# Performance work log

Measured on AMD Instinct MI355X. Metric: run time of the kernel, lower is better.

Reference implementation:

```python
import jax, jax.numpy as jnp
import numpy as np


def setup_inputs() -> dict:
    key = jax.random.key(0)
    ks = jax.random.split(key, 4)
    B, S, H = 1, 2048, 2048
    E, I = 32, 768
    scale_h = 1.0 / np.sqrt(H)
    scale_i = 1.0 / np.sqrt(I)
    return {
        "hidden_states": jax.random.normal(ks[0], (B, S, H), dtype=jnp.float32),
        "gate_w": jax.random.normal(ks[1], (E, H), dtype=jnp.float32) * scale_h,
        "gate_up_proj": jax.random.normal(ks[2], (E, H, 2 * I), dtype=jnp.float32) * scale_h,
        "down_proj": jax.random.normal(ks[3], (E, I, H), dtype=jnp.float32) * scale_i,
    }


TOP_K = 4


def reference(hidden_states, gate_w, gate_up_proj, down_proj):
    B, S, H = hidden_states.shape
    x = hidden_states.reshape(-1, H)                      # [T, H]
    T = x.shape[0]

    # Router: softmax -> top-k -> renormalize -> scatter back to dense [T, E]
    router_logits = x @ gate_w.T                          # [T, E]
    probs = jax.nn.softmax(router_logits.astype(jnp.float32), axis=-1)
    top_w, top_idx = jax.lax.top_k(probs, TOP_K)          # [T, K]
    top_w = top_w / jnp.sum(top_w, axis=-1, keepdims=True)
    top_w = top_w.astype(x.dtype)
    router_weights = jnp.zeros_like(router_logits).at[
        jnp.arange(T)[:, None], top_idx
    ].set(top_w)                                          # [T, E]

    # Experts (eval path): every expert processes every token, then weight & sum.
    gate_up = jnp.einsum("th,ehi->eti", x, gate_up_proj)  # [E, T, 2I]
    gate, up = jnp.split(gate_up, 2, axis=-1)
    h = up * jax.nn.silu(gate)                            # [E, T, I]
    expert_out = jnp.einsum("eti,eih->eth", h, down_proj)  # [E, T, H]
    out = jnp.einsum("eth,te->th", expert_out, router_weights)  # [T, H]

    return out.reshape(B, S, H), router_logits
```

## Files before the change

kernel.cpp:

```cpp
#include <hip/hip_runtime.h>
#include <hip/hip_bf16.h>

#define T_TOK 2048
#define H_DIM 2048
#define E_NUM 32
#define I_DIM 768
#define TOPK  4
#define S4    (T_TOK * TOPK)

typedef __attribute__((ext_vector_type(8))) short bf16x8;
typedef __attribute__((ext_vector_type(4))) float f32x4;

__device__ __forceinline__ unsigned pk2(float a, float b) {
    __hip_bfloat16 ha = __float2bfloat16(a);
    __hip_bfloat16 hb = __float2bfloat16(b);
    unsigned short ua = *(unsigned short*)&ha;
    unsigned short ub = *(unsigned short*)&hb;
    return (unsigned)ua | ((unsigned)ub << 16);
}

#define MFMA16(a, b, c) __builtin_amdgcn_mfma_f32_16x16x32_bf16(a, b, c, 0, 0, 0)

__global__ __launch_bounds__(64) void router_kernel(
    const float* __restrict__ x, const float* __restrict__ gate_w,
    float* __restrict__ logits_out, int* __restrict__ cnt,
    int* __restrict__ tok_list, float* __restrict__ tok_w,
    int* __restrict__ tok_slots)
{
    const int t = blockIdx.x;
    const int lane = threadIdx.x;
    __shared__ float xs[H_DIM];
    const float4* __restrict__ xv = (const float4*)(x + (size_t)t * H_DIM);
    float4* xsv = (float4*)xs;
#pragma unroll
    for (int i = 0; i < H_DIM / 4 / 64; ++i) xsv[lane + i * 64] = xv[lane + i * 64];
    __syncthreads();

    const int e = lane & 31;
    const int half = lane >> 5;
    const float4* __restrict__ wv = (const float4*)(gate_w + (size_t)e * H_DIM) + half * (H_DIM / 8);
    const float4* __restrict__ xh = ((const float4*)xs) + half * (H_DIM / 8);
    float acc = 0.f;
#pragma unroll 4
    for (int i = 0; i < H_DIM / 8; ++i) {
        float4 w4 = wv[i], x4 = xh[i];
        acc += w4.x * x4.x + w4.y * x4.y + w4.z * x4.z + w4.w * x4.w;
    }
    acc += __shfl_xor(acc, 32, 64);
    if (lane < 32) logits_out[(size_t)t * E_NUM + e] = acc;

    float v = acc;
    float topv[TOPK]; int topi[TOPK];
#pragma unroll
    for (int r = 0; r < TOPK; ++r) {
        float bv = v; int bi = e;
#pragma unroll
        for (int off = 16; off >= 1; off >>= 1) {
            float ov = __shfl_xor(bv, off, 32);
            int   oi = __shfl_xor(bi, off, 32);
            if (ov > bv || (ov == bv && oi < bi)) { bv = ov; bi = oi; }
        }
        topv[r] = bv; topi[r] = bi;
        if (e == bi) v = -1e30f;
    }
    if (lane == 0) {
        float w[TOPK]; float s = 0.f;
#pragma unroll
        for (int r = 0; r < TOPK; ++r) { w[r] = expf(topv[r] - topv[0]); s += w[r]; }
        float inv = 1.f / s;
#pragma unroll
        for (int r = 0; r < TOPK; ++r) {
            int pos = atomicAdd(&cnt[topi[r]], 1);
            tok_list[topi[r] * T_TOK + pos] = t;
            tok_w  [topi[r] * T_TOK + pos] = w[r] * inv;
            tok_slots[t * TOPK + r] = (topi[r] << 12) | pos;
        }
    }
}

__global__ void scan_kernel(const int* __restrict__ cnt, int* __restrict__ slot_base)
{
    if (threadIdx.x == 0) {
        int s = 0;
        for (int e = 0; e < E_NUM; ++e) { slot_base[e] = s; s += cnt[e]; }
        slot_base[E_NUM] = s;
    }
}

__global__ __launch_bounds__(256) void gather_kernel(
    const float* __restrict__ x, const int* __restrict__ cnt,
    const int* __restrict__ slot_base, const int* __restrict__ tok_list,
    unsigned short* __restrict__ xg_t)
{
    const int e = blockIdx.x;
    const int count = cnt[e];
    const int m0 = blockIdx.y * 8;
    if (m0 >= count) return;
    const int s8   = threadIdx.x >> 5;
    const int kc31 = threadIdx.x & 31;
    const int m = m0 + s8;
    if (m >= count) return;
    const int tok  = tok_list[e * T_TOK + m];
    const int slot = slot_base[e] + m;
    const float* __restrict__ src = x + (size_t)tok * H_DIM;
#pragma unroll
    for (int kcq = 0; kcq < 8; ++kcq) {
        const int kc = kcq * 32 + kc31;
        float4 a = *(const float4*)(src + kc * 8);
        float4 b = *(const float4*)(src + kc * 8 + 4);
        uint4 o;
        o.x = pk2(a.x, a.y); o.y = pk2(a.z, a.w);
        o.z = pk2(b.x, b.y); o.w = pk2(b.z, b.w);
        *(uint4*)(xg_t + ((size_t)kc * S4 + slot) * 8) = o;
    }
}

#define GU_NC (H_DIM / 128)
__global__ __launch_bounds__(512, 2) void gateup_mfma(
    const unsigned short* __restrict__ xg_t, const float* __restrict__ gup_w,
    const int* __restrict__ cnt, const int* __restrict__ slot_base,
    const float* __restrict__ tok_w, unsigned short* __restrict__ h_t)
{
    const int e  = blockIdx.x;
    const int nt = blockIdx.y;
    const int mt = blockIdx.z;
    const int count = cnt[e];
    if (mt * 256 >= count) return;
    const int tid  = threadIdx.x;
    const int lane = tid & 63;
    const int w    = tid >> 6;
    const int base = slot_base[e];
    const int l16  = lane & 15, lg = lane >> 4;

    __shared__ unsigned short Bls[2][2][16 * 32 * 8];
    __shared__ float wls[256];

    if (tid < 256) {
        int m = mt * 256 + tid; if (m >= count) m = count - 1;
        wls[tid] = tok_w[e * T_TOK + m];
    }

    int m0 = mt * 256 + w * 32 + l16;      if (m0 >= count) m0 = count - 1;
    int m1 = mt * 256 + w * 32 + 16 + l16; if (m1 >= count) m1 = count - 1;
    const unsigned short* a0b = xg_t + (size_t)(base + m0) * 8;
    const unsigned short* a1b = xg_t + (size_t)(base + m1) * 8;

    const int bhalf = tid >> 8;
    const int sub   = (tid >> 7) & 1;
    const int t7    = tid & 127;
    const int kb    = (t7 >> 3) * 2;
    const int n4    = (t7 & 7) * 4;
    const int k8    = kb & 7;
    const int kbh   = kb >> 3;
    const float* __restrict__ bbase =
        gup_w + ((size_t)e * H_DIM + kb) * (2 * I_DIM) + (size_t)bhalf * I_DIM + nt * 32 + n4;

    float4 sv0[2], sv1[2];
    bf16x8 aR[8];

#define GU_ALOAD(C) do { _Pragma("unroll") for (int s = 0; s < 4; ++s) { \
        const size_t ao_ = (size_t)((C) * 16 + s * 4 + lg) * (S4 * 8); \
        aR[s]     = *(const bf16x8*)(a0b + ao_); \
        aR[4 + s] = *(const bf16x8*)(a1b + ao_); } } while (0)
#define GU_LOAD(C) do { _Pragma("unroll") for (int q2 = 0; q2 < 2; ++q2) { \
        const int q = sub + q2 * 2; \
        const float* s_ = bbase + (size_t)((C) * 128 + q * 32) * (2 * I_DIM); \
        sv0[q2] = *(const float4*)s_; \
        sv1[q2] = *(const float4*)(s_ + 2 * I_DIM); } } while (0)
#define GU_WRITE(BUF) do { _Pragma("unroll") for (int q2 = 0; q2 < 2; ++q2) { \
        const int q = sub + q2 * 2; \
        unsigned short* bw_ = &Bls[BUF][bhalf][((q * 4 + kbh) * 32) * 8]; \
        float p0[4] = {sv0[q2].x, sv0[q2].y, sv0[q2].z, sv0[q2].w}; \
        float p1[4] = {sv1[q2].x, sv1[q2].y, sv1[q2].z, sv1[q2].w}; \
        _Pragma("unroll") for (int j = 0; j < 4; ++j) \
            *(unsigned*)&bw_[(n4 + j) * 8 + k8] = pk2(p0[j], p1[j]); } } while (0)

    f32x4 accg[2][2], accu[2][2];
#pragma unroll
    for (int i = 0; i < 2; ++i)
#pragma unroll
        for (int f = 0; f < 2; ++f) { accg[i][f] = {0.f,0.f,0.f,0.f}; accu[i][f] = {0.f,0.f,0.f,0.f}; }

    GU_LOAD(0);
    GU_WRITE(0);
    GU_ALOAD(0);

    for (int c = 0; c < GU_NC; ++c) {
        const int buf = c & 1;
        const bool pf = (c + 1 < GU_NC);
        __syncthreads();
        if (pf) GU_LOAD(c + 1);
#pragma unroll
        for (int s = 0; s < 4; ++s) {
            bf16x8 a0 = aR[s];
            bf16x8 a1 = aR[4 + s];
            if (pf) {
                const size_t ao_ = (size_t)((c + 1) * 16 + s * 4 + lg) * (S4 * 8);
                aR[s]     = *(const bf16x8*)(a0b + ao_);
                aR[4 + s] = *(const bf16x8*)(a1b + ao_);
            }
            const unsigned short* bg_ = &Bls[buf][0][((s * 4 + lg) * 32 + l16) * 8];
            const unsigned short* bu_ = &Bls[buf][1][((s * 4 + lg) * 32 + l16) * 8];
            bf16x8 g0 = *(const bf16x8*)(bg_);
            bf16x8 g1 = *(const bf16x8*)(bg_ + 128);
            bf16x8 u0 = *(const bf16x8*)(bu_);
            bf16x8 u1 = *(const bf16x8*)(bu_ + 128);
            accg[0][0] = MFMA16(a0, g0, accg[0][0]);
            accg[0][1] = MFMA16(a0, g1, accg[0][1]);
            accu[0][0] = MFMA16(a0, u0, accu[0][0]);
            accu[0][1] = MFMA16(a0, u1, accu[0][1]);
            accg[1][0] = MFMA16(a1, g0, accg[1][0]);
            accg[1][1] = MFMA16(a1, g1, accg[1][1]);
            accu[1][0] = MFMA16(a1, u0, accu[1][0]);
            accu[1][1] = MFMA16(a1, u1, accu[1][1]);
        }
        if (pf) GU_WRITE(buf ^ 1);
    }
#undef GU_ALOAD
#undef GU_LOAD
#undef GU_WRITE

#pragma unroll
    for (int i = 0; i < 2; ++i) {
        const int mloc = w * 32 + i * 16 + lg * 4;
#pragma unroll
        for (int r = 0; r < 4; ++r) {
            const int mrow = mt * 256 + mloc + r;
            if (mrow < count) {
                const float wgt = wls[mloc + r];
                const size_t slot = (size_t)(base + mrow);
#pragma unroll
                for (int f = 0; f < 2; ++f) {
                    const int col = nt * 32 + f * 16 + l16;
                    float g = accg[i][f][r], u = accu[i][f][r];
                    float sv = g / (1.f + expf(-g));
                    __hip_bfloat16 hb = __float2bfloat16(wgt * u * sv);
                    h_t[((size_t)(col >> 3) * S4 + slot) * 8 + (col & 7)] = *(unsigned short*)&hb;
                }
            }
        }
    }
}

#define DN_NC (I_DIM / 128)
__global__ __launch_bounds__(512, 2) void down_mfma(
    const unsigned short* __restrict__ h_t, const float* __restrict__ down_w,
    const int* __restrict__ cnt, const int* __restrict__ slot_base,
    float* __restrict__ ods)
{
    const int e  = blockIdx.x;
    const int nt = blockIdx.y;
    const int mt = blockIdx.z;
    const int count = cnt[e];
    if (mt * 256 >= count) return;
    const int tid  = threadIdx.x;
    const int lane = tid & 63;
    const int w    = tid >> 6;
    const int base = slot_base[e];
    const int l16  = lane & 15, lg = lane >> 4;

    __shared__ unsigned short Bls[2][16 * 64 * 8];

    int m0 = mt * 256 + w * 32 + l16;      if (m0 >= count) m0 = count - 1;
    int m1 = mt * 256 + w * 32 + 16 + l16; if (m1 >= count) m1 = count - 1;
    const unsigned short* a0b = h_t + (size_t)(base + m0) * 8;
    const unsigned short* a1b = h_t + (size_t)(base + m1) * 8;

    const int sub = tid >> 8;
    const int t8  = tid & 255;
    const int kb  = (t8 >> 4) * 2;
    const int n4  = (t8 & 15) * 4;
    const int k8  = kb & 7;
    const int kbh = kb >> 3;
    const float* __restrict__ bbase =
        down_w + ((size_t)e * I_DIM + kb) * H_DIM + nt * 64 + n4;

    float4 sv0[2], sv1[2];
    bf16x8 aR[8];

#define DN_ALOAD(C) do { _Pragma("unroll") for (int s = 0; s < 4; ++s) { \
        const size_t ao_ = (size_t)((C) * 16 + s * 4 + lg) * (S4 * 8); \
        aR[s]     = *(const bf16x8*)(a0b + ao_); \
        aR[4 + s] = *(const bf16x8*)(a1b + ao_); } } while (0)
#define DN_LOAD(C) do { _Pragma("unroll") for (int q2 = 0; q2 < 2; ++q2) { \
        const int q = sub + q2 * 2; \
        const float* s_ = bbase + (size_t)((C) * 128 + q * 32) * H_DIM; \
        sv0[q2] = *(const float4*)s_; \
        sv1[q2] = *(const float4*)(s_ + H_DIM); } } while (0)
#define DN_WRITE(BUF) do { _Pragma("unroll") for (int q2 = 0; q2 < 2; ++q2) { \
        const int q = sub + q2 * 2; \
        unsigned short* bw_ = &Bls[BUF][((q * 4 + kbh) * 64) * 8]; \
        float p0[4] = {sv0[q2].x, sv0[q2].y, sv0[q2].z, sv0[q2].w}; \
        float p1[4] = {sv1[q2].x, sv1[q2].y, sv1[q2].z, sv1[q2].w}; \
        _Pragma("unroll") for (int j = 0; j < 4; ++j) \
            *(unsigned*)&bw_[(n4 + j) * 8 + k8] = pk2(p0[j], p1[j]); } } while (0)

    f32x4 acc[2][4];
#pragma unroll
    for (int i = 0; i < 2; ++i)
#pragma unroll
        for (int f = 0; f < 4; ++f) acc[i][f] = {0.f,0.f,0.f,0.f};

    DN_LOAD(0);
    DN_WRITE(0);
    DN_ALOAD(0);

    for (int c = 0; c < DN_NC; ++c) {
        const int buf = c & 1;
        const bool pf = (c + 1 < DN_NC);
        __syncthreads();
        if (pf) DN_LOAD(c + 1);
#pragma unroll
        for (int s = 0; s < 4; ++s) {
            bf16x8 a0 = aR[s];
            bf16x8 a1 = aR[4 + s];
            if (pf) {
                const size_t ao_ = (size_t)((c + 1) * 16 + s * 4 + lg) * (S4 * 8);
                aR[s]     = *(const bf16x8*)(a0b + ao_);
                aR[4 + s] = *(const bf16x8*)(a1b + ao_);
            }
            const unsigned short* bf_ = &Bls[buf][((s * 4 + lg) * 64 + l16) * 8];
            bf16x8 b0 = *(const bf16x8*)(bf_);
            bf16x8 b1 = *(const bf16x8*)(bf_ + 128);
            bf16x8 b2 = *(const bf16x8*)(bf_ + 256);
            bf16x8 b3 = *(const bf16x8*)(bf_ + 384);
            acc[0][0] = MFMA16(a0, b0, acc[0][0]);
            acc[0][1] = MFMA16(a0, b1, acc[0][1]);
            acc[0][2] = MFMA16(a0, b2, acc[0][2]);
            acc[0][3] = MFMA16(a0, b3, acc[0][3]);
            acc[1][0] = MFMA16(a1, b0, acc[1][0]);
            acc[1][1] = MFMA16(a1, b1, acc[1][1]);
            acc[1][2] = MFMA16(a1, b2, acc[1][2]);
            acc[1][3] = MFMA16(a1, b3, acc[1][3]);
        }
        if (pf) DN_WRITE(buf ^ 1);
    }
#undef DN_ALOAD
#undef DN_LOAD
#undef DN_WRITE

#pragma unroll
    for (int i = 0; i < 2; ++i) {
        const int mloc = w * 32 + i * 16 + lg * 4;
#pragma unroll
        for (int r = 0; r < 4; ++r) {
            const int mrow = mt * 256 + mloc + r;
            if (mrow < count) {
                float* orow = ods + (size_t)(base + mrow) * H_DIM + nt * 64;
#pragma unroll
                for (int f = 0; f < 4; ++f)
                    orow[f * 16 + l16] = acc[i][f][r];
            }
        }
    }
}

__global__ __launch_bounds__(256) void combine_kernel(
    const float* __restrict__ ods, const int* __restrict__ tok_slots,
    const int* __restrict__ slot_base, float* __restrict__ out)
{
    const int t = blockIdx.x;
    const int c0 = threadIdx.x * 8;
    const float* rows[TOPK];
#pragma unroll
    for (int r = 0; r < TOPK; ++r) {
        const int pk = tok_slots[t * TOPK + r];
        const int e = pk >> 12, pos = pk & 4095;
        rows[r] = ods + (size_t)(slot_base[e] + pos) * H_DIM + c0;
    }
    float4 a0 = {0.f,0.f,0.f,0.f}, a1 = {0.f,0.f,0.f,0.f};
#pragma unroll
    for (int r = 0; r < TOPK; ++r) {
        float4 v0 = *(const float4*)(rows[r]);
        float4 v1 = *(const float4*)(rows[r] + 4);
        a0.x += v0.x; a0.y += v0.y; a0.z += v0.z; a0.w += v0.w;
        a1.x += v1.x; a1.y += v1.y; a1.z += v1.z; a1.w += v1.w;
    }
    float* o = out + (size_t)t * H_DIM + c0;
    *(float4*)o = a0;
    *(float4*)(o + 4) = a1;
}

extern "C" void kernel_launch(void* const* d_in, const int* in_sizes, int n_in,
                              void* d_out, int out_size, void* d_ws, size_t ws_size,
                              hipStream_t stream) {
    const float* x      = (const float*)d_in[0];
    const float* gate_w = (const float*)d_in[1];
    const float* gup_w  = (const float*)d_in[2];
    const float* down_w = (const float*)d_in[3];
    float* out    = (float*)d_out;

    char* wsp = (char*)d_ws;
    int*   cnt       = (int*)(wsp);
    int*   slot_base = (int*)(wsp + 256);
    int*   tok_list  = (int*)(wsp + 4096);
    float* tok_w     = (float*)(wsp + 4096 + (size_t)E_NUM * T_TOK * 4);
    int*   tok_slots = (int*)(wsp + (768u << 10));

    size_t off = (size_t)1 << 20;
    unsigned short* xg_t = (unsigned short*)(wsp + off); off += (size_t)S4 * H_DIM * 2;
    unsigned short* h_t  = (unsigned short*)(wsp + off); off += (size_t)S4 * I_DIM * 2;
    float*          ods  = (float*)(wsp + off);          off += (size_t)S4 * H_DIM * 4;

    hipMemsetAsync(cnt, 0, 256, stream);

    router_kernel<<<T_TOK, 64, 0, stream>>>(x, gate_w, out + (size_t)T_TOK * H_DIM,
                                            cnt, tok_list, tok_w, tok_slots);
    scan_kernel<<<1, 64, 0, stream>>>(cnt, slot_base);
    gather_kernel<<<dim3(E_NUM, 256), 256, 0, stream>>>(x, cnt, slot_base, tok_list, xg_t);
    gateup_mfma<<<dim3(E_NUM, 24, 8), 512, 0, stream>>>(
        xg_t, gup_w, cnt, slot_base, tok_w, h_t);
    down_mfma<<<dim3(E_NUM, 32, 8), 512, 0, stream>>>(
        h_t, down_w, cnt, slot_base, ods);
    combine_kernel<<<T_TOK, 256, 0, stream>>>(ods, tok_slots, slot_base, out);
}
```

Before: 443.2 us.

## Widen N tiles and shrink K chunks in expert GEMM kernels

Result: no change. 434.8 us (-1.9%).

```diff
diff --git a/kernel.cpp b/kernel.cpp
--- a/kernel.cpp
+++ b/kernel.cpp
@@ -115,7 +115,7 @@
     }
 }
 
-#define GU_NC (H_DIM / 128)
+#define GU_NC (H_DIM / 64)
 __global__ __launch_bounds__(512, 2) void gateup_mfma(
     const unsigned short* __restrict__ xg_t, const float* __restrict__ gup_w,
     const int* __restrict__ cnt, const int* __restrict__ slot_base,
@@ -132,7 +132,7 @@
     const int base = slot_base[e];
     const int l16  = lane & 15, lg = lane >> 4;
 
-    __shared__ unsigned short Bls[2][2][16 * 32 * 8];
+    __shared__ unsigned short Bls[2][2][4 * 192 * 8];
     __shared__ float wls[256];
 
     if (tid < 256) {
@@ -146,73 +146,62 @@
     const unsigned short* a1b = xg_t + (size_t)(base + m1) * 8;
 
     const int bhalf = tid >> 8;
-    const int sub   = (tid >> 7) & 1;
-    const int t7    = tid & 127;
-    const int kb    = (t7 >> 3) * 2;
-    const int n4    = (t7 & 7) * 4;
+    const int t8    = tid & 255;
+    const int kb    = (t8 >> 3) * 2;
+    const int n4    = (t8 & 7) * 4;
+    const int sq    = kb >> 5;
+    const int lgb   = (kb >> 3) & 3;
     const int k8    = kb & 7;
-    const int kbh   = kb >> 3;
     const float* __restrict__ bbase =
-        gup_w + ((size_t)e * H_DIM + kb) * (2 * I_DIM) + (size_t)bhalf * I_DIM + nt * 32 + n4;
-
-    float4 sv0[2], sv1[2];
-    bf16x8 aR[8];
-
-#define GU_ALOAD(C) do { _Pragma("unroll") for (int s = 0; s < 4; ++s) { \
-        const size_t ao_ = (size_t)((C) * 16 + s * 4 + lg) * (S4 * 8); \
+        gup_w + ((size_t)e * H_DIM + kb) * (2 * I_DIM) + (size_t)bhalf * I_DIM + nt * 96 + n4;
+
+    float4 sv0[3], sv1[3];
+    bf16x8 aR[4];
+
+#define GU_ALOAD(C) do { _Pragma("unroll") for (int s = 0; s < 2; ++s) { \
+        const size_t ao_ = (size_t)((C) * 8 + s * 4 + lg) * (S4 * 8); \
         aR[s]     = *(const bf16x8*)(a0b + ao_); \
-        aR[4 + s] = *(const bf16x8*)(a1b + ao_); } } while (0)
-#define GU_LOAD(C) do { _Pragma("unroll") for (int q2 = 0; q2 < 2; ++q2) { \
-        const int q = sub + q2 * 2; \
-        const float* s_ = bbase + (size_t)((C) * 128 + q * 32) * (2 * I_DIM); \
-        sv0[q2] = *(const float4*)s_; \
-        sv1[q2] = *(const float4*)(s_ + 2 * I_DIM); } } while (0)
-#define GU_WRITE(BUF) do { _Pragma("unroll") for (int q2 = 0; q2 < 2; ++q2) { \
-        const int q = sub + q2 * 2; \
-        unsigned short* bw_ = &Bls[BUF][bhalf][((q * 4 + kbh) * 32) * 8]; \
-        float p0[4] = {sv0[q2].x, sv0[q2].y, sv0[q2].z, sv0[q2].w}; \
-        float p1[4] = {sv1[q2].x, sv1[q2].y, sv1[q2].z, sv1[q2].w}; \
-        _Pragma("unroll") for (int j = 0; j < 4; ++j) \
-            *(unsigned*)&bw_[(n4 + j) * 8 + k8] = pk2(p0[j], p1[j]); } } while (0)
-
-    f32x4 accg[2][2], accu[2][2];
+        aR[2 + s] = *(const bf16x8*)(a1b + ao_); } } while (0)
+#define GU_LOAD(C) do { _Pragma("unroll") for (int j = 0; j < 3; ++j) { \
+        const float* s_ = bbase + (size_t)(C) * 64 * (2 * I_DIM) + j * 32; \
+        sv0[j] = *(const float4*)s_; \
+        sv1[j] = *(const float4*)(s_ + 2 * I_DIM); } } while (0)
+#define GU_WRITE(BUF) do { _Pragma("unroll") for (int j = 0; j < 3; ++j) { \
+        unsigned short* bw_ = &Bls[BUF][sq][(lgb * 192 + bhalf * 96 + j * 32 + n4) * 8 + k8]; \
+        float p0[4] = {sv0[j].x, sv0[j].y, sv0[j].z, sv0[j].w}; \
+        float p1[4] = {sv1[j].x, sv1[j].y, sv1[j].z, sv1[j].w}; \
+        _Pragma("unroll") for (int q = 0; q < 4; ++q) \
+            *(unsigned*)&bw_[q * 8] = pk2(p0[q], p1[q]); } } while (0)
+
+    f32x4 accg[2][6], accu[2][6];
 #pragma unroll
     for (int i = 0; i < 2; ++i)
 #pragma unroll
-        for (int f = 0; f < 2; ++f) { accg[i][f] = {0.f,0.f,0.f,0.f}; accu[i][f] = {0.f,0.f,0.f,0.f}; }
+        for (int f = 0; f < 6; ++f) { accg[i][f] = {0.f,0.f,0.f,0.f}; accu[i][f] = {0.f,0.f,0.f,0.f}; }
 
     GU_LOAD(0);
     GU_WRITE(0);
-    GU_ALOAD(0);
 
     for (int c = 0; c < GU_NC; ++c) {
         const int buf = c & 1;
         const bool pf = (c + 1 < GU_NC);
         __syncthreads();
+        GU_ALOAD(c);
         if (pf) GU_LOAD(c + 1);
 #pragma unroll
-        for (int s = 0; s < 4; ++s) {
+        for (int s = 0; s < 2; ++s) {
             bf16x8 a0 = aR[s];
-            bf16x8 a1 = aR[4 + s];
-            if (pf) {
-                const size_t ao_ = (size_t)((c + 1) * 16 + s * 4 + lg) * (S4 * 8);
-                aR[s]     = *(const bf16x8*)(a0b + ao_);
-                aR[4 + s] = *(const bf16x8*)(a1b + ao_);
+            bf16x8 a1 = aR[2 + s];
+            const unsigned short* bs_ = &Bls[buf][s][(lg * 192) * 8];
+#pragma unroll
+            for (int f = 0; f < 6; ++f) {
+                bf16x8 bg = *(const bf16x8*)(bs_ + (f * 16 + l16) * 8);
+                bf16x8 bu = *(const bf16x8*)(bs_ + (96 + f * 16 + l16) * 8);
+                accg[0][f] = MFMA16(a0, bg, accg[0][f]);
+                accg[1][f] = MFMA16(a1, bg, accg[1][f]);
+                accu[0][f] = MFMA16(a0, bu, accu[0][f]);
+                accu[1][f] = MFMA16(a1, bu, accu[1][f]);
             }
-            const unsigned short* bg_ = &Bls[buf][0][((s * 4 + lg) * 32 + l16) * 8];
-            const unsigned short* bu_ = &Bls[buf][1][((s * 4 + lg) * 32 + l16) * 8];
-            bf16x8 g0 = *(const bf16x8*)(bg_);
-            bf16x8 g1 = *(const bf16x8*)(bg_ + 128);
-            bf16x8 u0 = *(const bf16x8*)(bu_);
-            bf16x8 u1 = *(const bf16x8*)(bu_ + 128);
-            accg[0][0] = MFMA16(a0, g0, accg[0][0]);
-            accg[0][1] = MFMA16(a0, g1, accg[0][1]);
-            accu[0][0] = MFMA16(a0, u0, accu[0][0]);
-            accu[0][1] = MFMA16(a0, u1, accu[0][1]);
-            accg[1][0] = MFMA16(a1, g0, accg[1][0]);
-            accg[1][1] = MFMA16(a1, g1, accg[1][1]);
-            accu[1][0] = MFMA16(a1, u0, accu[1][0]);
-            accu[1][1] = MFMA16(a1, u1, accu[1][1]);
         }
         if (pf) GU_WRITE(buf ^ 1);
     }
@@ -230,8 +219,8 @@
                 const float wgt = wls[mloc + r];
                 const size_t slot = (size_t)(base + mrow);
 #pragma unroll
-                for (int f = 0; f < 2; ++f) {
-                    const int col = nt * 32 + f * 16 + l16;
+                for (int f = 0; f < 6; ++f) {
+                    const int col = nt * 96 + f * 16 + l16;
                     float g = accg[i][f][r], u = accu[i][f][r];
                     float sv = g / (1.f + expf(-g));
                     __hip_bfloat16 hb = __float2bfloat16(wgt * u * sv);
@@ -242,7 +231,7 @@
     }
 }
 
-#define DN_NC (I_DIM / 128)
+#define DN_NC (I_DIM / 32)
 __global__ __launch_bounds__(512, 2) void down_mfma(
     const unsigned short* __restrict__ h_t, const float* __restrict__ down_w,
     const int* __restrict__ cnt, const int* __restrict__ slot_base,
@@ -259,79 +248,63 @@
     const int base = slot_base[e];
     const int l16  = lane & 15, lg = lane >> 4;
 
-    __shared__ unsigned short Bls[2][16 * 64 * 8];
+    __shared__ unsigned short Bls[2][4 * 256 * 8];
 
     int m0 = mt * 256 + w * 32 + l16;      if (m0 >= count) m0 = count - 1;
     int m1 = mt * 256 + w * 32 + 16 + l16; if (m1 >= count) m1 = count - 1;
     const unsigned short* a0b = h_t + (size_t)(base + m0) * 8;
     const unsigned short* a1b = h_t + (size_t)(base + m1) * 8;
 
-    const int sub = tid >> 8;
-    const int t8  = tid & 255;
-    const int kb  = (t8 >> 4) * 2;
-    const int n4  = (t8 & 15) * 4;
+    const int kb  = (tid >> 5) * 2;
+    const int n4  = (tid & 31) * 4;
+    const int lgb = kb >> 3;
     const int k8  = kb & 7;
-    const int kbh = kb >> 3;
     const float* __restrict__ bbase =
-        down_w + ((size_t)e * I_DIM + kb) * H_DIM + nt * 64 + n4;
+        down_w + ((size_t)e * I_DIM + kb) * H_DIM + nt * 256 + n4;
 
     float4 sv0[2], sv1[2];
-    bf16x8 aR[8];
-
-#define DN_ALOAD(C) do { _Pragma("unroll") for (int s = 0; s < 4; ++s) { \
-        const size_t ao_ = (size_t)((C) * 16 + s * 4 + lg) * (S4 * 8); \
-        aR[s]     = *(const bf16x8*)(a0b + ao_); \
-        aR[4 + s] = *(const bf16x8*)(a1b + ao_); } } while (0)
-#define DN_LOAD(C) do { _Pragma("unroll") for (int q2 = 0; q2 < 2; ++q2) { \
-        const int q = sub + q2 * 2; \
-        const float* s_ = bbase + (size_t)((C) * 128 + q * 32) * H_DIM; \
-        sv0[q2] = *(const float4*)s_; \
-        sv1[q2] = *(const float4*)(s_ + H_DIM); } } while (0)
-#define DN_WRITE(BUF) do { _Pragma("unroll") for (int q2 = 0; q2 < 2; ++q2) { \
-        const int q = sub + q2 * 2; \
-        unsigned short* bw_ = &Bls[BUF][((q * 4 + kbh) * 64) * 8]; \
-        float p0[4] = {sv0[q2].x, sv0[q2].y, sv0[q2].z, sv0[q2].w}; \
-        float p1[4] = {sv1[q2].x, sv1[q2].y, sv1[q2].z, sv1[q2].w}; \
-        _Pragma("unroll") for (int j = 0; j < 4; ++j) \
-            *(unsigned*)&bw_[(n4 + j) * 8 + k8] = pk2(p0[j], p1[j]); } } while (0)
-
-    f32x4 acc[2][4];
+    bf16x8 aR[2];
+
+#define DN_ALOAD(C) do { \
+        const size_t ao_ = (size_t)((C) * 4 + lg) * (S4 * 8); \
+        aR[0] = *(const bf16x8*)(a0b + ao_); \
+        aR[1] = *(const bf16x8*)(a1b + ao_); } while (0)
+#define DN_LOAD(C) do { _Pragma("unroll") for (int j = 0; j < 2; ++j) { \
+        const float* s_ = bbase + (size_t)(C) * 32 * H_DIM + j * 128; \
+        sv0[j] = *(const float4*)s_; \
+        sv1[j] = *(const float4*)(s_ + H_DIM); } } while (0)
+#define DN_WRITE(BUF) do { _Pragma("unroll") for (int j = 0; j < 2; ++j) { \
+        unsigned short* bw_ = &Bls[BUF][(lgb * 256 + j * 128 + n4) * 8 + k8]; \
+        float p0[4] = {sv0[j].x, sv0[j].y, sv0[j].z, sv0[j].w}; \
+        float p1[4] = {sv1[j].x, sv1[j].y, sv1[j].z, sv1[j].w}; \
+        _Pragma("unroll") for (int q = 0; q < 4; ++q) \
+            *(unsigned*)&bw_[q * 8] = pk2(p0[q], p1[q]); } } while (0)
+
+    f32x4 acc[2][16];
 #pragma unroll
     for (int i = 0; i < 2; ++i)
 #pragma unroll
-        for (int f = 0; f < 4; ++f) acc[i][f] = {0.f,0.f,0.f,0.f};
+        for (int f = 0; f < 16; ++f) acc[i][f] = {0.f,0.f,0.f,0.f};
 
     DN_LOAD(0);
     DN_WRITE(0);
-    DN_ALOAD(0);
 
     for (int c = 0; c < DN_NC; ++c) {
         const int buf = c & 1;
         const bool pf = (c + 1 < DN_NC);
         __syncthreads();
+        DN_ALOAD(c);
         if (pf) DN_LOAD(c + 1);
-#pragma unroll
-        for (int s = 0; s < 4; ++s) {
-            bf16x8 a0 = aR[s];
-            bf16x8 a1 = aR[4 + s];
-            if (pf) {
-                const size_t ao_ = (size_t)((c + 1) * 16 + s * 4 + lg) * (S4 * 8);
-                aR[s]     = *(const bf16x8*)(a0b + ao_);
-                aR[4 + s] = *(const bf16x8*)(a1b + ao_);
+        {
+            bf16x8 a0 = aR[0];
+            bf16x8 a1 = aR[1];
+            const unsigned short* bs_ = &Bls[buf][(lg * 256) * 8];
+#pragma unroll
+            for (int f = 0; f < 16; ++f) {
+                bf16x8 b = *(const bf16x8*)(bs_ + (f * 16 + l16) * 8);
+                acc[0][f] = MFMA16(a0, b, acc[0][f]);
+                acc[1][f] = MFMA16(a1, b, acc[1][f]);
             }
-            const unsigned short* bf_ = &Bls[buf][((s * 4 + lg) * 64 + l16) * 8];
-            bf16x8 b0 = *(const bf16x8*)(bf_);
-            bf16x8 b1 = *(const bf16x8*)(bf_ + 128);
-            bf16x8 b2 = *(const bf16x8*)(bf_ + 256);
-            bf16x8 b3 = *(const bf16x8*)(bf_ + 384);
-            acc[0][0] = MFMA16(a0, b0, acc[0][0]);
-            acc[0][1] = MFMA16(a0, b1, acc[0][1]);
-            acc[0][2] = MFMA16(a0, b2, acc[0][2]);
-            acc[0][3] = MFMA16(a0, b3, acc[0][3]);
-            acc[1][0] = MFMA16(a1, b0, acc[1][0]);
-            acc[1][1] = MFMA16(a1, b1, acc[1][1]);
-            acc[1][2] = MFMA16(a1, b2, acc[1][2]);
-            acc[1][3] = MFMA16(a1, b3, acc[1][3]);
         }
         if (pf) DN_WRITE(buf ^ 1);
     }
@@ -346,9 +319,9 @@
         for (int r = 0; r < 4; ++r) {
             const int mrow = mt * 256 + mloc + r;
             if (mrow < count) {
-                float* orow = ods + (size_t)(base + mrow) * H_DIM + nt * 64;
-#pragma unroll
-                for (int f = 0; f < 4; ++f)
+                float* orow = ods + (size_t)(base + mrow) * H_DIM + nt * 256;
+#pragma unroll
+                for (int f = 0; f < 16; ++f)
                     orow[f * 16 + l16] = acc[i][f][r];
             }
         }
@@ -408,9 +381,9 @@
                                             cnt, tok_list, tok_w, tok_slots);
     scan_kernel<<<1, 64, 0, stream>>>(cnt, slot_base);
     gather_kernel<<<dim3(E_NUM, 256), 256, 0, stream>>>(x, cnt, slot_base, tok_list, xg_t);
-    gateup_mfma<<<dim3(E_NUM, 24, 8), 512, 0, stream>>>(
+    gateup_mfma<<<dim3(E_NUM, 8, 8), 512, 0, stream>>>(
         xg_t, gup_w, cnt, slot_base, tok_w, h_t);
-    down_mfma<<<dim3(E_NUM, 32, 8), 512, 0, stream>>>(
+    down_mfma<<<dim3(E_NUM, 8, 8), 512, 0, stream>>>(
         h_t, down_w, cnt, slot_base, ods);
     combine_kernel<<<T_TOK, 256, 0, stream>>>(ods, tok_slots, slot_base, out);
 }
```
